# Optimization experiments

Measured on AMD Instinct MI355X. Metric: run time of the kernel, lower is better.

Reference implementation:

```python
import jax, jax.numpy as jnp
import numpy as np

D_MODEL = 1024
NUM_HEADS = 16
D_K = D_MODEL // NUM_HEADS
C = 1.0  # Poincare ball curvature (MANIFOLD = PoincareBall(c=Curvature(1.0)))
EPS = 1e-15


def poincare_fully_connected(x, z, r, c):
    """hypll Poincare-ball fully connected layer (HNN++, Shimizu et al.).
    x: [..., in], z: [in, out], r: [out]. Returns a point in the ball, [..., out]."""
    c_sqrt = jnp.sqrt(c)
    lam = 2.0 / (1.0 - c * jnp.sum(x * x, axis=-1, keepdims=True))  # [..., 1]
    z_norm = jnp.maximum(jnp.linalg.norm(z, axis=0), EPS)  # [out]
    two_cr = 2.0 * c_sqrt * r  # [out]
    inner = x @ (z / z_norm)  # [..., out]
    # signed hyperplane distances v_k, then map back into the ball
    v = (2.0 * z_norm / c_sqrt) * jnp.arcsinh(
        c_sqrt * lam * inner * jnp.cosh(two_cr) - (lam - 1.0) * jnp.sinh(two_cr)
    )
    w = jnp.sinh(c_sqrt * v) / c_sqrt
    return w / (1.0 + jnp.sqrt(1.0 + c * jnp.sum(w * w, axis=-1, keepdims=True)))


def setup_inputs() -> dict:
    key = jax.random.key(0)
    ks = jax.random.split(key, 7)
    B, S, D = 4, 2048, D_MODEL
    x = jax.random.normal(ks[0], (B, S, D), jnp.float32)
    # place every token strictly inside the unit Poincare ball (max norm 0.7)
    x = 0.7 * x / jnp.max(jnp.linalg.norm(x, axis=-1, keepdims=True))
    scale = 1.0 / np.sqrt(D).astype(np.float32)
    return {
        "x": x,
        "z_q": jax.random.normal(ks[1], (D, D), jnp.float32) * scale,
        "b_q": jax.random.normal(ks[2], (D,), jnp.float32) * 0.01,
        "z_k": jax.random.normal(ks[3], (D, D), jnp.float32) * scale,
        "b_k": jax.random.normal(ks[4], (D,), jnp.float32) * 0.01,
        "w_v": jax.random.normal(ks[5], (D, D), jnp.float32) * scale,
        "b_v": jax.random.normal(ks[6], (D,), jnp.float32) * 0.01,
    }


def reference(x, z_q, b_q, z_k, b_k, w_v, b_v):
    B, S, D = x.shape
    Q = poincare_fully_connected(x, z_q, b_q, C)  # [B,S,D] hyperbolic projection
    K = poincare_fully_connected(x, z_k, b_k, C)  # [B,S,D]
    V = x @ w_v.T + b_v                            # [B,S,D] Euclidean nn.Linear

    def split_heads(t):  # [B,S,D] -> [B,H,S,Dk]
        return t.reshape(B, S, NUM_HEADS, D_K).transpose(0, 2, 1, 3)

    Qh, Kh, Vh = split_heads(Q), split_heads(K), split_heads(V)
    scores = jnp.einsum("bhqd,bhkd->bhqk", Qh, Kh) / np.sqrt(D_K).astype(np.float32)
    probs = jax.nn.softmax(scores, axis=-1)
    out = jnp.einsum("bhqk,bhkd->bhqd", probs, Vh)  # [B,H,S,Dk]
    return out.transpose(0, 2, 1, 3).reshape(B, S, D)
```

## Files before the change

### kernel.cpp

```cpp
#include <hip/hip_runtime.h>
#include <hip/hip_bf16.h>
#include <math.h>

#define D_MODEL 1024
#define NHEADS  16
#define DKH     64
#define BATCH   4
#define SEQ     2048
#define NTOK    (BATCH * SEQ)
#define NELEM   ((size_t)NTOK * D_MODEL)

typedef __bf16 v8bf __attribute__((ext_vector_type(8)));
typedef float  v4f  __attribute__((ext_vector_type(4)));

__device__ __forceinline__ v8bf ld_bf16x8(const ushort* p) {
    union { uint4 u; v8bf b; } cv;
    cv.u = *(const uint4*)p;
    return cv.b;
}
__device__ __forceinline__ ushort f2bf(float f) {
    __hip_bfloat16 h = __float2bfloat16(f);
    return *(ushort*)&h;
}
__device__ __forceinline__ uint cvt_pk_bf16(float lo, float hi) {
    uint r;
    asm("v_cvt_pk_bf16_f32 %0, %1, %2" : "=v"(r) : "v"(lo), "v"(hi));
    return r;
}

#define GLOAD_LDS16(gsrc, ldst)                                            \
    __builtin_amdgcn_global_load_lds(                                      \
        (const __attribute__((address_space(1))) void*)(gsrc),             \
        (__attribute__((address_space(3))) void*)(ldst), 16, 0, 0)

#define RAW_BARRIER() __builtin_amdgcn_s_barrier()

__device__ __forceinline__ float block_reduce_sum(float v, float* sbuf) {
    #pragma unroll
    for (int off = 32; off > 0; off >>= 1)
        v += __shfl_xor(v, off, 64);
    int lane = threadIdx.x & 63;
    int wid  = threadIdx.x >> 6;
    if (lane == 0) sbuf[wid] = v;
    __syncthreads();
    float total = sbuf[0] + sbuf[1] + sbuf[2] + sbuf[3];
    __syncthreads();
    return total;
}

__global__ __launch_bounds__(256) void prep_kernel2(const float* __restrict__ z_q,
                                                    const float* __restrict__ r_q,
                                                    const float* __restrict__ z_k,
                                                    const float* __restrict__ r_k,
                                                    float* __restrict__ aux) {
    __shared__ float sbuf[4];
    const float* z = blockIdx.y ? z_k : z_q;
    const float* r = blockIdx.y ? r_k : r_q;
    float* base = aux + blockIdx.y * 3072;
    int m = blockIdx.x;
    float s = 0.f;
    for (int k = threadIdx.x; k < D_MODEL; k += 256) {
        float zv = z[k * D_MODEL + m];
        s += zv * zv;
    }
    float tot = block_reduce_sum(s, sbuf);
    if (threadIdx.x == 0) {
        float n = fmaxf(sqrtf(tot), 1e-15f);
        float tc = 2.f * r[m];
        base[m]        = coshf(tc) / n;
        base[1024 + m] = sinhf(tc);
        base[2048 + m] = 2.f * n;
    }
}

__global__ __launch_bounds__(256) void cast_x_lam(const float* __restrict__ x,
                                                  ushort* __restrict__ xb,
                                                  float* __restrict__ lam) {
    __shared__ float sbuf[4];
    int n = blockIdx.x;
    const float* xr = x + (size_t)n * D_MODEL;
    float4 v = *(const float4*)&xr[threadIdx.x * 4];
    float s = v.x * v.x + v.y * v.y + v.z * v.z + v.w * v.w;
    float xn2 = block_reduce_sum(s, sbuf);
    if (threadIdx.x == 0) lam[n] = 2.f / (1.f - xn2);
    ushort u[4] = {f2bf(v.x), f2bf(v.y), f2bf(v.z), f2bf(v.w)};
    *(uint2*)&xb[(size_t)n * D_MODEL + threadIdx.x * 4] = *(uint2*)u;
}

__global__ __launch_bounds__(256) void cast_bf16(const float* __restrict__ in,
                                                 ushort* __restrict__ out) {
    size_t i = ((size_t)blockIdx.x * 256 + threadIdx.x) * 8;
    float4 a = *(const float4*)(in + i);
    float4 b = *(const float4*)(in + i + 4);
    ushort u[8] = {f2bf(a.x), f2bf(a.y), f2bf(a.z), f2bf(a.w),
                   f2bf(b.x), f2bf(b.y), f2bf(b.z), f2bf(b.w)};
    *(uint4*)(out + i) = *(uint4*)u;
}

__global__ __launch_bounds__(256) void cast_transpose2(const float* __restrict__ zq,
                                                       const float* __restrict__ zk,
                                                       ushort* __restrict__ zqT,
                                                       ushort* __restrict__ zkT) {
    __shared__ float tile[64][65];
    const float* z = blockIdx.z ? zk : zq;
    ushort* zT = blockIdx.z ? zkT : zqT;
    int t = threadIdx.x;
    int k0 = blockIdx.y * 64, m0 = blockIdx.x * 64;
    #pragma unroll
    for (int i = 0; i < 4; ++i) {
        int r = (t >> 4) + 16 * i;
        int c = (t & 15) * 4;
        float4 v = *(const float4*)&z[(size_t)(k0 + r) * D_MODEL + m0 + c];
        tile[r][c + 0] = v.x; tile[r][c + 1] = v.y;
        tile[r][c + 2] = v.z; tile[r][c + 3] = v.w;
    }
    __syncthreads();
    #pragma unroll
    for (int i = 0; i < 2; ++i) {
        int idx = t + 256 * i;
        int r = idx >> 3;
        int c8 = idx & 7;
        ushort u[8];
        #pragma unroll
        for (int j = 0; j < 8; ++j)
            u[j] = f2bf(tile[c8 * 8 + j][r]);
        *(uint4*)&zT[(size_t)(m0 + r) * D_MODEL + k0 + c8 * 8] = *(uint4*)u;
    }
}

__global__ __launch_bounds__(256) void gemm_fused(const ushort* __restrict__ A,
                                                  const ushort* __restrict__ W,
                                                  const float* __restrict__ bias,
                                                  ushort* __restrict__ Pq,
                                                  ushort* __restrict__ Pk,
                                                  ushort* __restrict__ VT) {
    const int K = 1024;
    __shared__ ushort As[2][128][64];
    __shared__ ushort Bs[2][128][64];
    int tid = threadIdx.x;
    int w = tid >> 6, l = tid & 63;
    int lr = l & 15, lg = l >> 4;
    int wr = w >> 1, wc = w & 1;
    int bid = blockIdx.x;
    int xcd = bid & 7, t = bid >> 3;
    int m0 = (xcd * 8 + ((t >> 2) & 7)) * 128;
    int n0 = ((t >> 5) * 4 + (t & 3)) * 128;

    v4f acc[4][4];
    #pragma unroll
    for (int i = 0; i < 4; ++i)
        #pragma unroll
        for (int j = 0; j < 4; ++j)
            acc[i][j] = (v4f){0.f, 0.f, 0.f, 0.f};

    int srow = w * 32 + (l >> 3);
    int scol = (l & 7) * 8;

#define STAGE_G(buf, k0) do {                                                 \
        _Pragma("unroll")                                                     \
        for (int j = 0; j < 4; ++j) {                                         \
            GLOAD_LDS16(A + (size_t)(m0 + srow + j * 8) * K + (k0) + scol,    \
                        &As[buf][w * 32 + j * 8][0]);                         \
            GLOAD_LDS16(W + (size_t)(n0 + srow + j * 8) * K + (k0) + scol,    \
                        &Bs[buf][w * 32 + j * 8][0]);                         \
        }                                                                     \
    } while (0)

    STAGE_G(0, 0);
    for (int k0 = 0; k0 < K; k0 += 64) {
        int cur = (k0 >> 6) & 1;
        if (k0 + 64 < K) {
            STAGE_G(cur ^ 1, k0 + 64);
            asm volatile("s_waitcnt vmcnt(8)" ::: "memory");
        } else {
            asm volatile("s_waitcnt vmcnt(0)" ::: "memory");
        }
        RAW_BARRIER();
        #pragma unroll
        for (int kk = 0; kk < 2; ++kk) {
            v8bf av[4], bv[4];
            #pragma unroll
            for (int i = 0; i < 4; ++i)
                av[i] = *(const v8bf*)&As[cur][wr * 64 + i * 16 + lr][kk * 32 + lg * 8];
            #pragma unroll
            for (int j = 0; j < 4; ++j)
                bv[j] = *(const v8bf*)&Bs[cur][wc * 64 + j * 16 + lr][kk * 32 + lg * 8];
            #pragma unroll
            for (int i = 0; i < 4; ++i)
                #pragma unroll
                for (int j = 0; j < 4; ++j)
                    acc[i][j] = __builtin_amdgcn_mfma_f32_16x16x32_bf16(av[i], bv[j], acc[i][j], 0, 0, 0);
        }
        RAW_BARRIER();
    }
#undef STAGE_G

    int chunk = n0 >> 10;
    #pragma unroll
    for (int i = 0; i < 4; ++i) {
        #pragma unroll
        for (int j = 0; j < 4; ++j) {
            int col = n0 + wc * 64 + j * 16 + lr;
            int cl  = col & 1023;
            if (chunk < 2) {
                ushort* P = chunk ? Pk : Pq;
                #pragma unroll
                for (int reg = 0; reg < 4; ++reg) {
                    int row = m0 + wr * 64 + i * 16 + 4 * lg + reg;
                    P[(size_t)row * D_MODEL + cl] = f2bf(acc[i][j][reg]);
                }
            } else {
                float badd = bias[cl];
                int hh = cl >> 6, dk = cl & 63;
                int row = m0 + wr * 64 + i * 16 + 4 * lg;
                int bb = row >> 11, ss = row & 2047;
                int sp = (ss & ~63) | (ss & 0x23) | ((ss & 0x0C) << 1) | ((ss & 0x10) >> 2);
                ushort u[4];
                #pragma unroll
                for (int reg = 0; reg < 4; ++reg)
                    u[reg] = f2bf(acc[i][j][reg] + badd);
                *(uint2*)&VT[(((size_t)(bb * NHEADS + hh)) * DKH + dk) * SEQ + sp] = *(uint2*)u;
            }
        }
    }
}

__global__ __launch_bounds__(256) void poincare_epilogue2(const ushort* __restrict__ Pq,
                                                          const ushort* __restrict__ Pk,
                                                          const float* __restrict__ lam_,
                                                          const float* __restrict__ aux,
                                                          ushort* __restrict__ Qb,
                                                          ushort* __restrict__ Kb) {
    __shared__ float sbuf[4];
    int which = blockIdx.y;
    const ushort* P  = which ? Pk : Pq;
    ushort* outb     = which ? Kb : Qb;
    const float* c1_ = aux + which * 3072;
    const float* sh_ = c1_ + 1024;
    const float* tz_ = c1_ + 2048;
    float oscale = which ? 1.0f : 0.1803368801f;

    int n = blockIdx.x;
    float lam = lam_[n];
    float lm1 = lam - 1.f;
    int o = threadIdx.x * 4;
    uint2 pu = *(const uint2*)&P[(size_t)n * D_MODEL + o];
    float4 c1 = *(const float4*)&c1_[o];
    float4 sh = *(const float4*)&sh_[o];
    float4 tz = *(const float4*)&tz_[o];
    float pv[4];
    pv[0] = __uint_as_float(pu.x << 16);
    pv[1] = __uint_as_float(pu.x & 0xffff0000u);
    pv[2] = __uint_as_float(pu.y << 16);
    pv[3] = __uint_as_float(pu.y & 0xffff0000u);
    float c1v[4] = {c1.x, c1.y, c1.z, c1.w};
    float shv[4] = {sh.x, sh.y, sh.z, sh.w};
    float tzv[4] = {tz.x, tz.y, tz.z, tz.w};
    float w[4];
    float wn2 = 0.f;
    #pragma unroll
    for (int i = 0; i < 4; ++i) {
        float t  = fmaf(lam * c1v[i], pv[i], -lm1 * shv[i]);
        float at = fabsf(t);
        float u  = at + __builtin_amdgcn_sqrtf(fmaf(at, at, 1.f));
        float tl = tzv[i] * __builtin_amdgcn_logf(u);
        float e  = __builtin_amdgcn_exp2f(tl);
        float em = __builtin_amdgcn_exp2f(-tl);
        float wa = 0.5f * (e - em);
        w[i] = copysignf(wa, t);
        wn2 = fmaf(wa, wa, wn2);
    }
    wn2 = block_reduce_sum(wn2, sbuf);
    float invd = oscale / (1.f + __builtin_amdgcn_sqrtf(1.f + wn2));
    uint2 st;
    st.x = cvt_pk_bf16(w[0] * invd, w[1] * invd);
    st.y = cvt_pk_bf16(w[2] * invd, w[3] * invd);
    *(uint2*)&outb[(size_t)n * D_MODEL + o] = st;
}

__global__ __launch_bounds__(512, 4) void attn_mfma(const ushort* __restrict__ Qb,
                                                    const ushort* __restrict__ Kb,
                                                    const ushort* __restrict__ VT,
                                                    float* __restrict__ Out) {
    __shared__ ushort Klds[4][64 * 64];
    __shared__ ushort Vlds[4][64 * 64];

    int tid = threadIdx.x;
    int w = tid >> 6, l = tid & 63;
    int lr = l & 15, lg = l >> 4;

    int flat = blockIdx.x;
    int low3 = flat & 7;
    int rest = flat >> 3;
    int qx   = rest & 7;
    int g    = (rest & ~7) | low3;
    int h = g & 15, b = g >> 4;

    const ushort* Kh = Kb + (size_t)b * SEQ * D_MODEL + h * DKH;
    const ushort* Vh = VT + (size_t)(b * NHEADS + h) * DKH * SEQ;

    const ushort* qp0 = Qb + (size_t)b * SEQ * D_MODEL + h * DKH
                      + (size_t)(qx * 256 + w * 32 + lr) * D_MODEL;
    const ushort* qp1 = qp0 + (size_t)16 * D_MODEL;
    v8bf qa[2][2];
    qa[0][0] = ld_bf16x8(qp0 + lg * 8);
    qa[0][1] = ld_bf16x8(qp0 + 32 + lg * 8);
    qa[1][0] = ld_bf16x8(qp1 + lg * 8);
    qa[1][1] = ld_bf16x8(qp1 + 32 + lg * 8);

    int row = tid >> 3;
    int c8  = (tid & 7) ^ (row & 7);
    const ushort* kg = Kh + (size_t)row * D_MODEL + c8 * 8;
    const ushort* vg = Vh + (size_t)row * SEQ + c8 * 8;

#define STAGE_KV(buf, st)  do {                                              \
        GLOAD_LDS16(kg + (size_t)(st) * 64 * D_MODEL, &Klds[buf][tid * 8]);  \
        GLOAD_LDS16(vg + (st) * 64, &Vlds[buf][tid * 8]);                    \
    } while (0)

    v4f o[2][4];
    v4f den4[2];
    #pragma unroll
    for (int st = 0; st < 2; ++st) {
        den4[st] = (v4f){0.f, 0.f, 0.f, 0.f};
        #pragma unroll
        for (int i = 0; i < 4; ++i) o[st][i] = (v4f){0.f, 0.f, 0.f, 0.f};
    }
    union { uint u[4]; v8bf v; } ones;
    ones.u[0] = ones.u[1] = ones.u[2] = ones.u[3] = 0x3f803f80u;

    auto compute = [&](int buf) {
        const char* Kc = (const char*)&Klds[buf][0];
        const char* Vc = (const char*)&Vlds[buf][0];

        v4f sc[2][4];
        #pragma unroll
        for (int st = 0; st < 2; ++st)
            #pragma unroll
            for (int i = 0; i < 4; ++i) sc[st][i] = (v4f){0.f, 0.f, 0.f, 0.f};
        __builtin_amdgcn_s_setprio(1);
        #pragma unroll
        for (int f = 0; f < 2; ++f) {
            #pragma unroll
            for (int sub = 0; sub < 4; ++sub) {
                int key = sub * 16 + lr;
                v8bf kb = *(const v8bf*)(Kc + key * 128 +
                                         ((f * 64 + lg * 16) ^ ((key & 7) << 4)));
                sc[0][sub] = __builtin_amdgcn_mfma_f32_16x16x32_bf16(kb, qa[0][f], sc[0][sub], 0, 0, 0);
                sc[1][sub] = __builtin_amdgcn_mfma_f32_16x16x32_bf16(kb, qa[1][f], sc[1][sub], 0, 0, 0);
            }
        }
        __builtin_amdgcn_s_setprio(0);

        uint pk[2][8];
        #pragma unroll
        for (int st = 0; st < 2; ++st) {
            #pragma unroll
            for (int sub = 0; sub < 4; ++sub) {
                float p0 = __builtin_amdgcn_exp2f(sc[st][sub][0]);
                float p1 = __builtin_amdgcn_exp2f(sc[st][sub][1]);
                float p2 = __builtin_amdgcn_exp2f(sc[st][sub][2]);
                float p3 = __builtin_amdgcn_exp2f(sc[st][sub][3]);
                pk[st][sub * 2 + 0] = cvt_pk_bf16(p0, p1);
                pk[st][sub * 2 + 1] = cvt_pk_bf16(p2, p3);
            }
        }

        __builtin_amdgcn_s_setprio(1);
        #pragma unroll
        for (int f = 0; f < 2; ++f) {
            union { uint u[4]; v8bf v; } pa0, pa1;
            #pragma unroll
            for (int j = 0; j < 4; ++j) { pa0.u[j] = pk[0][4 * f + j]; pa1.u[j] = pk[1][4 * f + j]; }
            den4[0] = __builtin_amdgcn_mfma_f32_16x16x32_bf16(pa0.v, ones.v, den4[0], 0, 0, 0);
            den4[1] = __builtin_amdgcn_mfma_f32_16x16x32_bf16(pa1.v, ones.v, den4[1], 0, 0, 0);
            #pragma unroll
            for (int sub = 0; sub < 4; ++sub) {
                int dk = sub * 16 + lr;
                v8bf vb = *(const v8bf*)(Vc + dk * 128 +
                                         ((f * 64 + lg * 16) ^ ((dk & 7) << 4)));
                o[0][sub] = __builtin_amdgcn_mfma_f32_16x16x32_bf16(pa0.v, vb, o[0][sub], 0, 0, 0);
                o[1][sub] = __builtin_amdgcn_mfma_f32_16x16x32_bf16(pa1.v, vb, o[1][sub], 0, 0, 0);
            }
        }
        __builtin_amdgcn_s_setprio(0);
    };

    STAGE_KV(0, 0);
    STAGE_KV(1, 1);
    STAGE_KV(2, 2);

    for (int tb = 0; tb < 28; tb += 4) {
        #pragma unroll
        for (int i = 0; i < 4; ++i) {
            asm volatile("s_waitcnt vmcnt(4)" ::: "memory");
            RAW_BARRIER();
            STAGE_KV((i + 3) & 3, tb + i + 3);
            compute(i);
        }
    }
    asm volatile("s_waitcnt vmcnt(4)" ::: "memory");
    RAW_BARRIER();
    STAGE_KV(3, 31);
    compute(0);
    asm volatile("s_waitcnt vmcnt(4)" ::: "memory");
    RAW_BARRIER();
    compute(1);
    asm volatile("s_waitcnt vmcnt(2)" ::: "memory");
    RAW_BARRIER();
    compute(2);
    asm volatile("s_waitcnt vmcnt(0)" ::: "memory");
    RAW_BARRIER();
    compute(3);

    #pragma unroll
    for (int st = 0; st < 2; ++st) {
        size_t obase = (size_t)b * SEQ * D_MODEL +
                       (size_t)(qx * 256 + w * 32 + st * 16 + lg * 4) * D_MODEL + h * DKH;
        #pragma unroll
        for (int reg = 0; reg < 4; ++reg) {
            float inv = 1.f / den4[st][reg];
            #pragma unroll
            for (int sub = 0; sub < 4; ++sub)
                Out[obase + (size_t)reg * D_MODEL + sub * 16 + lr] = o[st][sub][reg] * inv;
        }
    }
#undef STAGE_KV
}

extern "C" void kernel_launch(void* const* d_in, const int* in_sizes, int n_in,
                              void* d_out, int out_size, void* d_ws, size_t ws_size,
                              hipStream_t stream) {
    const float* x   = (const float*)d_in[0];
    const float* z_q = (const float*)d_in[1];
    const float* b_q = (const float*)d_in[2];
    const float* z_k = (const float*)d_in[3];
    const float* b_k = (const float*)d_in[4];
    const float* w_v = (const float*)d_in[5];
    const float* b_v = (const float*)d_in[6];
    float* out = (float*)d_out;

    ushort* Pq   = (ushort*)d_ws;
    ushort* xb   = Pq + NELEM;
    ushort* Qb   = xb;
    ushort* Wcat = xb + NELEM;
    ushort* VT   = Wcat + (size_t)3 * D_MODEL * D_MODEL;
    ushort* Kb   = VT + NELEM;
    float*  aux  = (float*)(Kb + NELEM);
    float*  lam  = aux + 6144;
    ushort* Pk   = (ushort*)out;

    prep_kernel2<<<dim3(1024, 2), 256, 0, stream>>>(z_q, b_q, z_k, b_k, aux);

    cast_x_lam<<<dim3(NTOK), 256, 0, stream>>>(x, xb, lam);
    cast_transpose2<<<dim3(16, 16, 2), 256, 0, stream>>>(z_q, z_k, Wcat,
                                                         Wcat + (size_t)D_MODEL * D_MODEL);
    cast_bf16<<<dim3(D_MODEL * D_MODEL / 8 / 256), 256, 0, stream>>>(
        w_v, Wcat + (size_t)2 * D_MODEL * D_MODEL);

    gemm_fused<<<dim3(1536), 256, 0, stream>>>(xb, Wcat, b_v, Pq, Pk, VT);

    poincare_epilogue2<<<dim3(NTOK, 2), 256, 0, stream>>>(Pq, Pk, lam, aux, Qb, Kb);

    attn_mfma<<<dim3(512), 512, 0, stream>>>(Qb, Kb, VT, out);
}
```

Baseline: 187.5 us.

## Use 4-stage K=32 pipeline with XOR-swizzled LDS in fused projection GEMM

```diff
diff --git a/kernel.cpp b/kernel.cpp
--- a/kernel.cpp
+++ b/kernel.cpp
@@ -135,8 +135,8 @@
                                                   ushort* __restrict__ Pk,
                                                   ushort* __restrict__ VT) {
     const int K = 1024;
-    __shared__ ushort As[2][128][64];
-    __shared__ ushort Bs[2][128][64];
+    __shared__ ushort As[4][128 * 32];
+    __shared__ ushort Bs[4][128 * 32];
     int tid = threadIdx.x;
     int w = tid >> 6, l = tid & 63;
     int lr = l & 15, lg = l >> 4;
@@ -153,46 +153,63 @@
         for (int j = 0; j < 4; ++j)
             acc[i][j] = (v4f){0.f, 0.f, 0.f, 0.f};
 
-    int srow = w * 32 + (l >> 3);
-    int scol = (l & 7) * 8;
-
-#define STAGE_G(buf, k0) do {                                                 \
-        _Pragma("unroll")                                                     \
-        for (int j = 0; j < 4; ++j) {                                         \
-            GLOAD_LDS16(A + (size_t)(m0 + srow + j * 8) * K + (k0) + scol,    \
-                        &As[buf][w * 32 + j * 8][0]);                         \
-            GLOAD_LDS16(W + (size_t)(n0 + srow + j * 8) * K + (k0) + scol,    \
-                        &Bs[buf][w * 32 + j * 8][0]);                         \
-        }                                                                     \
+    int arow = tid >> 2;
+    int achk = (tid & 3) ^ ((arow >> 1) & 3);
+    const ushort* Ab = A + (size_t)(m0 + arow) * K + achk * 8;
+    const ushort* Wb = W + (size_t)(n0 + arow) * K + achk * 8;
+
+#define STAGE_G(buf, st) do {                                                  \
+        GLOAD_LDS16(Ab + (size_t)(st) * 32,             &As[buf][tid * 8]);    \
+        GLOAD_LDS16(Ab + (size_t)64 * K + (st) * 32,    &As[buf][(tid + 256) * 8]); \
+        GLOAD_LDS16(Wb + (size_t)(st) * 32,             &Bs[buf][tid * 8]);    \
+        GLOAD_LDS16(Wb + (size_t)64 * K + (st) * 32,    &Bs[buf][(tid + 256) * 8]); \
     } while (0)
 
+    int swzr = (lg ^ ((lr >> 1) & 3)) << 4;
+
+    auto compute = [&](int buf) {
+        v8bf av[4], bv[4];
+        #pragma unroll
+        for (int i = 0; i < 4; ++i)
+            av[i] = *(const v8bf*)((const char*)&As[buf][0]
+                                   + (wr * 64 + i * 16 + lr) * 64 + swzr);
+        #pragma unroll
+        for (int j = 0; j < 4; ++j)
+            bv[j] = *(const v8bf*)((const char*)&Bs[buf][0]
+                                   + (wc * 64 + j * 16 + lr) * 64 + swzr);
+        #pragma unroll
+        for (int i = 0; i < 4; ++i)
+            #pragma unroll
+            for (int j = 0; j < 4; ++j)
+                acc[i][j] = __builtin_amdgcn_mfma_f32_16x16x32_bf16(av[i], bv[j], acc[i][j], 0, 0, 0);
+    };
+
     STAGE_G(0, 0);
-    for (int k0 = 0; k0 < K; k0 += 64) {
-        int cur = (k0 >> 6) & 1;
-        if (k0 + 64 < K) {
-            STAGE_G(cur ^ 1, k0 + 64);
+    STAGE_G(1, 1);
+    STAGE_G(2, 2);
+
+    for (int tb = 0; tb < 28; tb += 4) {
+        #pragma unroll
+        for (int i = 0; i < 4; ++i) {
             asm volatile("s_waitcnt vmcnt(8)" ::: "memory");
-        } else {
-            asm volatile("s_waitcnt vmcnt(0)" ::: "memory");
-        }
-        RAW_BARRIER();
-        #pragma unroll
-        for (int kk = 0; kk < 2; ++kk) {
-            v8bf av[4], bv[4];
-            #pragma unroll
-            for (int i = 0; i < 4; ++i)
-                av[i] = *(const v8bf*)&As[cur][wr * 64 + i * 16 + lr][kk * 32 + lg * 8];
-            #pragma unroll
-            for (int j = 0; j < 4; ++j)
-                bv[j] = *(const v8bf*)&Bs[cur][wc * 64 + j * 16 + lr][kk * 32 + lg * 8];
-            #pragma unroll
-            for (int i = 0; i < 4; ++i)
-                #pragma unroll
-                for (int j = 0; j < 4; ++j)
-                    acc[i][j] = __builtin_amdgcn_mfma_f32_16x16x32_bf16(av[i], bv[j], acc[i][j], 0, 0, 0);
-        }
-        RAW_BARRIER();
-    }
+            RAW_BARRIER();
+            STAGE_G((i + 3) & 3, tb + i + 3);
+            compute(i);
+        }
+    }
+    asm volatile("s_waitcnt vmcnt(8)" ::: "memory");
+    RAW_BARRIER();
+    STAGE_G(3, 31);
+    compute(0);
+    asm volatile("s_waitcnt vmcnt(8)" ::: "memory");
+    RAW_BARRIER();
+    compute(1);
+    asm volatile("s_waitcnt vmcnt(4)" ::: "memory");
+    RAW_BARRIER();
+    compute(2);
+    asm volatile("s_waitcnt vmcnt(0)" ::: "memory");
+    RAW_BARRIER();
+    compute(3);
 #undef STAGE_G
 
     int chunk = n0 >> 10;
```

Result: faster. 183.5 us (-2.1%).
